# Optimization experiments

Hardware: AMD Instinct MI355X
Metric: run time of the kernel (lower is better)

Reference implementation:

```python
import jax, jax.numpy as jnp
import numpy as np

WS = (7, 7, 7)
SS = (3, 3, 3)
SEQ = WS[0] * WS[1] * WS[2]  # 343
EPS = 1e-5


def layer_norm(x, w, b):
    mu = jnp.mean(x, axis=-1, keepdims=True)
    var = jnp.mean((x - mu) ** 2, axis=-1, keepdims=True)
    return (x - mu) * jax.lax.rsqrt(var + EPS) * w + b


def window_partition(x, ws):
    b, d, h, w, c = x.shape
    x = x.reshape(b, d // ws[0], ws[0], h // ws[1], ws[1], w // ws[2], ws[2], c)
    return x.transpose(0, 1, 3, 5, 2, 4, 6, 7).reshape(-1, ws[0] * ws[1] * ws[2], c)


def window_reverse(win, ws, dims):
    b, dp, hp, wp = dims
    x = win.reshape(b, dp // ws[0], hp // ws[1], wp // ws[2], ws[0], ws[1], ws[2], -1)
    return x.transpose(0, 1, 4, 2, 5, 3, 6, 7).reshape(b, dp, hp, wp, -1)


def _rel_pos_index():
    coords = np.stack(np.meshgrid(np.arange(WS[0]), np.arange(WS[1]), np.arange(WS[2]), indexing='ij'))
    cf = coords.reshape(3, -1)
    rel = (cf[:, :, None] - cf[:, None, :]).transpose(1, 2, 0)  # (s, s, 3)
    rel[..., 0] += WS[0] - 1
    rel[..., 1] += WS[1] - 1
    rel[..., 2] += WS[2] - 1
    idx = rel[..., 0] * (2 * WS[1] - 1) * (2 * WS[2] - 1) + rel[..., 1] * (2 * WS[2] - 1) + rel[..., 2]
    return idx.astype(np.int32)


def _swin_mask(dp, hp, wp):
    img = np.zeros((1, dp, hp, wp, 1), np.float32)
    cnt = 0
    sl = lambda ws, ss: (slice(0, -ws), slice(-ws, -ss), slice(-ss, None))
    for ds in sl(WS[0], SS[0]):
        for hs in sl(WS[1], SS[1]):
            for wsl in sl(WS[2], SS[2]):
                img[:, ds, hs, wsl, :] = cnt
                cnt += 1
    mw = np.asarray(window_partition(jnp.asarray(img), WS)).squeeze(-1)  # (nW, s)
    am = mw[:, None, :] - mw[:, :, None]
    return np.where(am != 0, np.float32(-100.0), np.float32(0.0))


def setup_inputs() -> dict:
    key = jax.random.key(0)
    ks = jax.random.split(key, 12)
    B, D, H, W, C = 1, 28, 56, 28, 192
    NH, DH = 6, 32
    FFI = 4 * C
    L = 2
    s = 0.02
    inp = {
        'x': jax.random.normal(ks[0], (B, D, H, W, C), jnp.float32),
        'mask_matrix': jnp.asarray(_swin_mask(D, H, W)),
        'clinical': jax.random.normal(ks[1], (B, 8), jnp.float32),
        'ln1_w': jnp.ones((L, C)), 'ln1_b': jnp.zeros((L, C)),
        'qkv_w': jax.random.normal(ks[2], (L, C, 3 * C)) * s, 'qkv_b': jnp.zeros((L, 3 * C)),
        'out_w': jax.random.normal(ks[3], (L, C, C)) * s, 'out_b': jnp.zeros((L, C)),
        'ln2_w': jnp.ones((L, C)), 'ln2_b': jnp.zeros((L, C)),
        'ff1_w': jax.random.normal(ks[4], (L, C, 2 * FFI)) * s, 'ff1_b': jnp.zeros((L, 2 * FFI)),
        'ff2_w': jax.random.normal(ks[5], (L, FFI, C)) * s, 'ff2_b': jnp.zeros((L, C)),
        'rpb': jax.random.normal(ks[6], (L, (2 * WS[0] - 1) * (2 * WS[1] - 1) * (2 * WS[2] - 1), NH)) * s,
        'lnf_w': jnp.ones((C,)), 'lnf_b': jnp.zeros((C,)),
        'rel_index': jnp.asarray(_rel_pos_index()),
    }
    return inp


def reference(x, mask_matrix, clinical, ln1_w, ln1_b, qkv_w, qkv_b, out_w, out_b,
              ln2_w, ln2_b, ff1_w, ff1_b, ff2_w, ff2_b, rpb, lnf_w, lnf_b, rel_index):
    b, d, h, w, c = x.shape
    nh = rpb.shape[-1]
    dh = c // nh
    # pad to window multiples (no-op for chosen shapes, kept for fidelity)
    pd = (WS[0] - d % WS[0]) % WS[0]
    ph = (WS[1] - h % WS[1]) % WS[1]
    pw = (WS[2] - w % WS[2]) % WS[2]
    xp = jnp.pad(x, ((0, 0), (0, pd), (0, ph), (0, pw), (0, 0)))
    dp, hp, wp = d + pd, h + ph, w + pw
    # cyclic shift
    xs = jnp.roll(xp, shift=(-SS[0], -SS[1], -SS[2]), axis=(1, 2, 3))
    xw = window_partition(xs, WS)  # (nW*b, s, c)
    # mask: values {0,-100} -> allowed bool (True = attend), per source math
    allowed = jnp.logical_not((mask_matrix * (-1.0 / 100.0)).astype(bool))[:, None, :, :]
    scale = 1.0 / jnp.sqrt(jnp.asarray(dh, xw.dtype))
    for l in range(2):
        hdn = layer_norm(xw, ln1_w[l], ln1_b[l])
        qkv = hdn @ qkv_w[l] + qkv_b[l]
        q, k, v = jnp.split(qkv, 3, axis=-1)
        q = q.reshape(-1, SEQ, nh, dh).transpose(0, 2, 1, 3)
        k = k.reshape(-1, SEQ, nh, dh).transpose(0, 2, 1, 3)
        v = v.reshape(-1, SEQ, nh, dh).transpose(0, 2, 1, 3)
        scores = jnp.einsum('whqd,whkd->whqk', q, k) * scale
        bias = rpb[l][rel_index].transpose(2, 0, 1)  # (nh, s, s)
        scores = scores + bias[None]
        scores = jnp.where(allowed, scores, jnp.asarray(-1e9, scores.dtype))
        attn = jax.nn.softmax(scores, axis=-1)
        o = jnp.einsum('whqk,whkd->whqd', attn, v).transpose(0, 2, 1, 3).reshape(-1, SEQ, c)
        xw = xw + (o @ out_w[l] + out_b[l])
        f = layer_norm(xw, ln2_w[l], ln2_b[l]) @ ff1_w[l] + ff1_b[l]
        u, g = jnp.split(f, 2, axis=-1)  # GLU feed-forward
        xw = xw + ((u * jax.nn.gelu(g)) @ ff2_w[l] + ff2_b[l])
    xw = layer_norm(xw, lnf_w, lnf_b)
    aw = xw.reshape(-1, WS[0], WS[1], WS[2], c)
    xs = window_reverse(aw, WS, (b, dp, hp, wp))
    xo = jnp.roll(xs, shift=(SS[0], SS[1], SS[2]), axis=(1, 2, 3))
    return xo[:, :d, :h, :w, :]
```

## Files before the change

kernel.cpp:

```cpp
#include <hip/hip_runtime.h>
#include <hip/hip_fp16.h>
#include <math.h>

#define SEQ 343
#define CCH 192
#define NWIN 128
#define NHEAD 6
#define TOK (NWIN * SEQ)

typedef __bf16 bf16x8 __attribute__((ext_vector_type(8)));
typedef float f32x4 __attribute__((ext_vector_type(4)));
typedef unsigned short ushort8 __attribute__((ext_vector_type(8)));
typedef _Float16 half8 __attribute__((ext_vector_type(8)));
typedef _Float16 half4 __attribute__((ext_vector_type(4)));

__device__ __forceinline__ unsigned short f2bf(float f) {
    unsigned u = __float_as_uint(f);
    u += 0x7FFF + ((u >> 16) & 1);
    return (unsigned short)(u >> 16);
}

__device__ __forceinline__ float gelu_tanh(float x) {
    const float k0 = 0.7978845608028654f;
    const float k1 = 0.044715f;
    float t = tanhf(k0 * (x + k1 * x * x * x));
    return 0.5f * x * (1.0f + t);
}

__global__ __launch_bounds__(256) void k_shift_part(const float* __restrict__ x,
                                                    float* __restrict__ xw) {
    int idx = blockIdx.x * 256 + threadIdx.x;
    if (idx >= TOK * 48) return;
    int c4 = idx % 48;
    int tok = idx / 48;
    int t = tok % SEQ;
    int wn = tok / SEQ;
    int tw = t % 7, th = (t / 7) % 7, td = t / 49;
    int ww = wn & 3, wh = (wn >> 2) & 7, wd = wn >> 5;
    int sd = (wd * 7 + td + 3) % 28;
    int sh = (wh * 7 + th + 3) % 56;
    int sw = (ww * 7 + tw + 3) % 28;
    const float4* src = (const float4*)(x + (size_t)((sd * 56 + sh) * 28 + sw) * CCH);
    ((float4*)xw)[idx] = src[c4];
}

__global__ __launch_bounds__(256) void k_ln_bf(const float* __restrict__ in,
                                               const float* __restrict__ w,
                                               const float* __restrict__ b,
                                               unsigned short* __restrict__ out, int rows) {
    int row = blockIdx.x * 4 + (threadIdx.x >> 6);
    int lane = threadIdx.x & 63;
    if (row >= rows) return;
    const float* p = in + (size_t)row * CCH;
    float v0 = p[lane], v1 = p[lane + 64], v2 = p[lane + 128];
    float s = v0 + v1 + v2;
#pragma unroll
    for (int off = 32; off > 0; off >>= 1) s += __shfl_xor(s, off);
    float mu = s * (1.0f / 192.0f);
    float d0 = v0 - mu, d1 = v1 - mu, d2 = v2 - mu;
    float vv = d0 * d0 + d1 * d1 + d2 * d2;
#pragma unroll
    for (int off = 32; off > 0; off >>= 1) vv += __shfl_xor(vv, off);
    float rs = rsqrtf(vv * (1.0f / 192.0f) + 1e-5f);
    unsigned short* q = out + (size_t)row * CCH;
    q[lane] = f2bf(d0 * rs * w[lane] + b[lane]);
    q[lane + 64] = f2bf(d1 * rs * w[lane + 64] + b[lane + 64]);
    q[lane + 128] = f2bf(d2 * rs * w[lane + 128] + b[lane + 128]);
}

__global__ __launch_bounds__(256) void k_ln_out(const float* __restrict__ xw,
                                                const float* __restrict__ w,
                                                const float* __restrict__ b,
                                                float* __restrict__ out) {
    int row = blockIdx.x * 4 + (threadIdx.x >> 6);
    int lane = threadIdx.x & 63;
    if (row >= TOK) return;
    int d = row / 1568;
    int hh = (row / 28) % 56;
    int wv = row % 28;
    int sd = (d + 25) % 28, sh = (hh + 53) % 56, sw = (wv + 25) % 28;
    int wn = (sd / 7) * 32 + (sh / 7) * 4 + (sw / 7);
    int t = (sd % 7) * 49 + (sh % 7) * 7 + (sw % 7);
    const float* p = xw + ((size_t)wn * SEQ + t) * CCH;
    float v0 = p[lane], v1 = p[lane + 64], v2 = p[lane + 128];
    float s = v0 + v1 + v2;
#pragma unroll
    for (int off = 32; off > 0; off >>= 1) s += __shfl_xor(s, off);
    float mu = s * (1.0f / 192.0f);
    float d0 = v0 - mu, d1 = v1 - mu, d2 = v2 - mu;
    float vv = d0 * d0 + d1 * d1 + d2 * d2;
#pragma unroll
    for (int off = 32; off > 0; off >>= 1) vv += __shfl_xor(vv, off);
    float rs = rsqrtf(vv * (1.0f / 192.0f) + 1e-5f);
    float* q = out + (size_t)row * CCH;
    q[lane] = d0 * rs * w[lane] + b[lane];
    q[lane + 64] = d1 * rs * w[lane + 64] + b[lane + 64];
    q[lane + 128] = d2 * rs * w[lane + 128] + b[lane + 128];
}

__global__ __launch_bounds__(256) void k_wprep(const float* __restrict__ qkv_w,
                                               const float* __restrict__ out_w,
                                               const float* __restrict__ ff1_w,
                                               const float* __restrict__ ff2_w,
                                               unsigned short* __restrict__ wt) {
    int idx = blockIdx.x * 256 + threadIdx.x;
    if (idx >= 1179648) return;
    int l = idx / 589824;
    int r = idx - l * 589824;
    const float* src;
    int Kd, Nd, off;
    if (r < 110592)      { src = qkv_w + (size_t)l * 110592; Kd = 192; Nd = 576;  off = r; }
    else if (r < 147456) { src = out_w + (size_t)l * 36864;  Kd = 192; Nd = 192;  off = r - 110592; }
    else if (r < 442368) { src = ff1_w + (size_t)l * 294912; Kd = 192; Nd = 1536; off = r - 147456; }
    else                 { src = ff2_w + (size_t)l * 147456; Kd = 768; Nd = 192;  off = r - 442368; }
    int n = off / Kd, k = off - n * Kd;
    wt[idx] = f2bf(src[(size_t)k * Nd + n]);
}

__global__ void k_cbgen2(const float* __restrict__ mask, const float* __restrict__ rpb,
                         unsigned* __restrict__ cb) {
    int q = threadIdx.x;
    int kp = blockIdx.x;
    int h = blockIdx.y;
    int cl = blockIdx.z;
    int wn = ((cl & 4) ? 96 : 0) + ((cl & 2) ? 28 : 0) + ((cl & 1) ? 3 : 0);
    const float LOG2E = 1.4426950408889634f;
    int qd = q / 49, qh = (q / 7) % 7, qw = q % 7;
    unsigned short v[2];
#pragma unroll
    for (int t = 0; t < 2; ++t) {
        int k = 2 * kp + t;
        float val = -14000.0f;
        if (k < SEQ && q < SEQ) {
            float mk = mask[((size_t)wn * SEQ + k) * SEQ + q];
            if (mk == 0.0f) {
                int kd = k / 49, kh = (k / 7) % 7, kw = k % 7;
                int rel = (qd - kd + 6) * 169 + (qh - kh + 6) * 13 + (qw - kw + 6);
                val = rpb[(size_t)rel * NHEAD + h] * LOG2E;
            }
        }
        v[t] = __half_as_ushort(__float2half_rn(val));
    }
    cb[((size_t)(cl * NHEAD + h) * 176 + kp) * 352 + q] = (unsigned)v[0] | ((unsigned)v[1] << 16);
}

template <int MODE>
__global__ __launch_bounds__(256) void k_gemm_mfma(const unsigned short* __restrict__ A,
                                                   const unsigned short* __restrict__ Wt,
                                                   const float* __restrict__ bias,
                                                   float* __restrict__ outF,
                                                   unsigned short* __restrict__ outB,
                                                   _Float16* __restrict__ outH,
                                                   _Float16* __restrict__ outV,
                                                   int N, int K) {
    __shared__ unsigned short As[128][72];
    __shared__ unsigned short Bs[64][72];
    __shared__ unsigned short Bs2[(MODE == 2) ? 64 : 1][72];
    const int tid = threadIdx.x;
    const int n0 = blockIdx.x * 64;
    const size_t m0 = (size_t)blockIdx.y * 128;
    const int lane = tid & 63, wid = tid >> 6;
    const int wr = wid >> 1, wc = wid & 1;
    f32x4 acc[4][2];
    f32x4 acc2[4][2];
#pragma unroll
    for (int m = 0; m < 4; ++m)
#pragma unroll
        for (int n = 0; n < 2; ++n) {
            acc[m][n] = (f32x4){0.f, 0.f, 0.f, 0.f};
            acc2[m][n] = (f32x4){0.f, 0.f, 0.f, 0.f};
        }
    const int arow = wr * 64 + (lane & 15);
    const int bcol = wc * 32 + (lane & 15);
    const int kg = (lane >> 4) * 8;
    for (int kb = 0; kb < K; kb += 64) {
#pragma unroll
        for (int i = 0; i < 4; ++i) {
            int idx = tid + i * 256;
            int r = idx >> 3, ck = (idx & 7) << 3;
            *(ushort8*)&As[r][ck] = *(const ushort8*)&A[(m0 + r) * (size_t)K + kb + ck];
        }
#pragma unroll
        for (int i = 0; i < 2; ++i) {
            int idx = tid + i * 256;
            int r = idx >> 3, ck = (idx & 7) << 3;
            *(ushort8*)&Bs[r][ck] = *(const ushort8*)&Wt[(size_t)(n0 + r) * K + kb + ck];
            if (MODE == 2)
                *(ushort8*)&Bs2[r][ck] = *(const ushort8*)&Wt[(size_t)(N + n0 + r) * K + kb + ck];
        }
        __syncthreads();
#pragma unroll
        for (int kk = 0; kk < 64; kk += 32) {
            bf16x8 a[4], b[2];
#pragma unroll
            for (int m = 0; m < 4; ++m) a[m] = *(const bf16x8*)&As[arow + m * 16][kk + kg];
#pragma unroll
            for (int n = 0; n < 2; ++n) b[n] = *(const bf16x8*)&Bs[bcol + n * 16][kk + kg];
#pragma unroll
            for (int m = 0; m < 4; ++m)
#pragma unroll
                for (int n = 0; n < 2; ++n)
                    acc[m][n] = __builtin_amdgcn_mfma_f32_16x16x32_bf16(a[m], b[n], acc[m][n], 0, 0, 0);
            if (MODE == 2) {
                bf16x8 b2[2];
#pragma unroll
                for (int n = 0; n < 2; ++n) b2[n] = *(const bf16x8*)&Bs2[bcol + n * 16][kk + kg];
#pragma unroll
                for (int m = 0; m < 4; ++m)
#pragma unroll
                    for (int n = 0; n < 2; ++n)
                        acc2[m][n] = __builtin_amdgcn_mfma_f32_16x16x32_bf16(a[m], b2[n], acc2[m][n], 0, 0, 0);
            }
        }
        __syncthreads();
    }
    const float S2LOG = 0.17677669529663687f * 1.4426950408889634f;
    const int col0 = n0 + wc * 32 + (lane & 15);
    const int row0 = (int)m0 + wr * 64 + ((lane >> 4) << 2);
#pragma unroll
    for (int n = 0; n < 2; ++n) {
        int gc = col0 + n * 16;
        float bb = bias[gc];
        float bg = (MODE == 2) ? bias[N + gc] : 0.f;
#pragma unroll
        for (int m = 0; m < 4; ++m) {
            int gr = row0 + m * 16;
#pragma unroll
            for (int j = 0; j < 4; ++j) {
                float v = acc[m][n][j] + bb;
                size_t o = (size_t)(gr + j) * N + gc;
                if (MODE == 1) {
                    outF[o] += v;
                } else if (MODE == 2) {
                    float g = acc2[m][n][j] + bg;
                    outB[o] = f2bf(v * gelu_tanh(g));
                } else {
                    int rr = gr + j;
                    if (gc < 384) {
                        outH[(size_t)rr * 384 + gc] = (_Float16)(gc < 192 ? v * S2LOG : v);
                    } else {
                        int d = gc - 384;
                        int hh = d >> 5, dd = d & 31;
                        int wn_ = rr / 343, qq = rr - wn_ * 343;
                        outV[(((size_t)wn_ * NHEAD + hh) * 32 + dd) * 344 + qq] = (_Float16)v;
                    }
                }
            }
        }
    }
}

__global__ __launch_bounds__(256) void k_attn3(const _Float16* __restrict__ qk,
                                               const _Float16* __restrict__ vt,
                                               const unsigned* __restrict__ cb,
                                               unsigned short* __restrict__ o) {
    __shared__ _Float16 Ks[352][40];
    __shared__ _Float16 Vt[32][360];
    __shared__ _Float16 Pb[4][48][16][4];
    const int h = blockIdx.x;
    const int wn = blockIdx.y;
    const int tid = threadIdx.x;
    const _Float16* kbase = qk + (size_t)wn * SEQ * 384 + 192 + h * 32;
    for (int j = tid; j < 352 * 4; j += 256) {
        int s = j >> 2, c = (j & 3) * 8;
        half8 v = {};
        if (s < SEQ) v = *(const half8*)&kbase[(size_t)s * 384 + c];
        *(half8*)&Ks[s][c] = v;
    }
    const _Float16* vbase = vt + ((size_t)wn * NHEAD + h) * 32 * 344;
    for (int j = tid; j < 32 * 44; j += 256) {
        int d = j / 44, c = (j % 44) * 8;
        half8 v = {};
        if (c + 7 <= 342) {
            v = *(const half8*)&vbase[(size_t)d * 344 + c];
        } else if (c <= 342) {
#pragma unroll
            for (int i = 0; i < 8; ++i) v[i] = (c + i <= 342) ? vbase[(size_t)d * 344 + c + i] : (_Float16)0.f;
        }
        *(half8*)&Vt[d][c] = v;
    }
    __syncthreads();
    const int wid = tid >> 6, lane = tid & 63;
    const int qloc = lane & 15, g = lane >> 4;
    int cls = (((wn >> 5) == 3) ? 4 : 0) | ((((wn >> 2) & 7) == 7) ? 2 : 0) | (((wn & 3) == 3) ? 1 : 0);
    const unsigned* cbb = cb + (size_t)(cls * NHEAD + h) * 176 * 352;
    for (int qt = wid; qt < 22; qt += 4) {
        const int q0 = qt * 16;
        const int qrow = q0 + qloc;
        half8 qf = {};
        if (qrow < SEQ) qf = *(const half8*)&qk[((size_t)wn * SEQ + qrow) * 384 + h * 32 + g * 8];
        f32x4 st[22];
#pragma unroll
        for (int kt = 0; kt < 22; ++kt) {
            half8 kf = *(const half8*)&Ks[kt * 16 + qloc][g * 8];
            st[kt] = __builtin_amdgcn_mfma_f32_16x16x32_f16(kf, qf, (f32x4){0.f, 0.f, 0.f, 0.f}, 0, 0, 0);
        }
        float m = -1e30f;
#pragma unroll
        for (int kt = 0; kt < 22; ++kt) {
            const unsigned* cp = cbb + (size_t)(kt * 8 + g * 2) * 352 + q0 + qloc;
            unsigned b0 = cp[0];
            unsigned b1 = cp[352];
            __half2 h0 = *(__half2*)&b0, h1 = *(__half2*)&b1;
            st[kt][0] += __low2float(h0);
            st[kt][1] += __high2float(h0);
            st[kt][2] += __low2float(h1);
            st[kt][3] += __high2float(h1);
            m = fmaxf(m, fmaxf(fmaxf(st[kt][0], st[kt][1]), fmaxf(st[kt][2], st[kt][3])));
        }
        m = fmaxf(m, __shfl_xor(m, 16));
        m = fmaxf(m, __shfl_xor(m, 32));
        float l = 0.f;
        f32x4 acc0 = {0.f, 0.f, 0.f, 0.f}, acc1 = {0.f, 0.f, 0.f, 0.f};
        asm volatile("s_waitcnt lgkmcnt(0)" ::: "memory");
#pragma unroll
        for (int kt = 0; kt < 12; ++kt) {
            float p0 = exp2f(st[kt][0] - m), p1 = exp2f(st[kt][1] - m);
            float p2 = exp2f(st[kt][2] - m), p3 = exp2f(st[kt][3] - m);
            l += (p0 + p1) + (p2 + p3);
            half4 pv = {(_Float16)p0, (_Float16)p1, (_Float16)p2, (_Float16)p3};
            *(half4*)&Pb[wid][kt * 4 + g][qloc][0] = pv;
        }
        asm volatile("s_waitcnt lgkmcnt(0)" ::: "memory");
#pragma unroll
        for (int ks = 0; ks < 6; ++ks) {
            half4 pa = *(half4*)&Pb[wid][ks * 8 + g * 2][qloc][0];
            half4 pb = *(half4*)&Pb[wid][ks * 8 + g * 2 + 1][qloc][0];
            half8 pf = {pa[0], pa[1], pa[2], pa[3], pb[0], pb[1], pb[2], pb[3]};
            half8 v0 = *(const half8*)&Vt[qloc][ks * 32 + g * 8];
            half8 v1 = *(const half8*)&Vt[16 + qloc][ks * 32 + g * 8];
            acc0 = __builtin_amdgcn_mfma_f32_16x16x32_f16(v0, pf, acc0, 0, 0, 0);
            acc1 = __builtin_amdgcn_mfma_f32_16x16x32_f16(v1, pf, acc1, 0, 0, 0);
        }
        asm volatile("s_waitcnt lgkmcnt(0)" ::: "memory");
#pragma unroll
        for (int kt = 12; kt < 22; ++kt) {
            float p0 = exp2f(st[kt][0] - m), p1 = exp2f(st[kt][1] - m);
            float p2 = exp2f(st[kt][2] - m), p3 = exp2f(st[kt][3] - m);
            l += (p0 + p1) + (p2 + p3);
            half4 pv = {(_Float16)p0, (_Float16)p1, (_Float16)p2, (_Float16)p3};
            *(half4*)&Pb[wid][(kt - 12) * 4 + g][qloc][0] = pv;
        }
        asm volatile("s_waitcnt lgkmcnt(0)" ::: "memory");
#pragma unroll
        for (int ks = 0; ks < 5; ++ks) {
            half4 pa = *(half4*)&Pb[wid][ks * 8 + g * 2][qloc][0];
            half4 pb = *(half4*)&Pb[wid][ks * 8 + g * 2 + 1][qloc][0];
            half8 pf = {pa[0], pa[1], pa[2], pa[3], pb[0], pb[1], pb[2], pb[3]};
            half8 v0 = *(const half8*)&Vt[qloc][192 + ks * 32 + g * 8];
            half8 v1 = *(const half8*)&Vt[16 + qloc][192 + ks * 32 + g * 8];
            acc0 = __builtin_amdgcn_mfma_f32_16x16x32_f16(v0, pf, acc0, 0, 0, 0);
            acc1 = __builtin_amdgcn_mfma_f32_16x16x32_f16(v1, pf, acc1, 0, 0, 0);
        }
        l += __shfl_xor(l, 16);
        l += __shfl_xor(l, 32);
        if (qrow < SEQ) {
            float inv = 1.0f / l;
            unsigned short* orow = o + ((size_t)wn * SEQ + qrow) * CCH + h * 32;
            ushort2 w0 = {f2bf(acc0[0] * inv), f2bf(acc0[1] * inv)};
            ushort2 w1 = {f2bf(acc0[2] * inv), f2bf(acc0[3] * inv)};
            ushort2 w2 = {f2bf(acc1[0] * inv), f2bf(acc1[1] * inv)};
            ushort2 w3 = {f2bf(acc1[2] * inv), f2bf(acc1[3] * inv)};
            *(ushort2*)&orow[g * 4] = w0;
            *(ushort2*)&orow[g * 4 + 2] = w1;
            *(ushort2*)&orow[16 + g * 4] = w2;
            *(ushort2*)&orow[16 + g * 4 + 2] = w3;
        }
    }
}

extern "C" void kernel_launch(void* const* d_in, const int* in_sizes, int n_in,
                              void* d_out, int out_size, void* d_ws, size_t ws_size,
                              hipStream_t stream) {
    const float* x     = (const float*)d_in[0];
    const float* mask  = (const float*)d_in[1];
    const float* ln1_w = (const float*)d_in[3];
    const float* ln1_b = (const float*)d_in[4];
    const float* qkv_w = (const float*)d_in[5];
    const float* qkv_b = (const float*)d_in[6];
    const float* out_w = (const float*)d_in[7];
    const float* out_b = (const float*)d_in[8];
    const float* ln2_w = (const float*)d_in[9];
    const float* ln2_b = (const float*)d_in[10];
    const float* ff1_w = (const float*)d_in[11];
    const float* ff1_b = (const float*)d_in[12];
    const float* ff2_w = (const float*)d_in[13];
    const float* ff2_b = (const float*)d_in[14];
    const float* rpb   = (const float*)d_in[15];
    const float* lnf_w = (const float*)d_in[16];
    const float* lnf_b = (const float*)d_in[17];

    char* wsp = (char*)d_ws;
    float* xw = (float*)wsp;                          wsp += (size_t)TOK * 192 * 4;
    unsigned short* hdnb = (unsigned short*)wsp;      wsp += (size_t)TOK * 192 * 2;
    _Float16* qkh = (_Float16*)wsp;                   wsp += (size_t)TOK * 384 * 2;
    _Float16* vth = (_Float16*)wsp;                   wsp += (size_t)NWIN * NHEAD * 32 * 344 * 2;
    unsigned short* glub = (unsigned short*)wsp;      wsp += (size_t)TOK * 768 * 2;
    unsigned short* wt = (unsigned short*)wsp;        wsp += (size_t)1179648 * 2;
    unsigned* cb = (unsigned*)wsp;
    float* out = (float*)d_out;

    k_shift_part<<<8232, 256, 0, stream>>>(x, xw);
    k_wprep<<<4608, 256, 0, stream>>>(qkv_w, out_w, ff1_w, ff2_w, wt);
    for (int l = 0; l < 2; ++l) {
        unsigned short* wbase = wt + (size_t)l * 589824;
        k_cbgen2<<<dim3(176, NHEAD, 8), 352, 0, stream>>>(mask, rpb + (size_t)l * 2197 * NHEAD, cb);
        k_ln_bf<<<10976, 256, 0, stream>>>(xw, ln1_w + l * 192, ln1_b + l * 192, hdnb, TOK);
        k_gemm_mfma<3><<<dim3(9, 343), 256, 0, stream>>>(hdnb, wbase, qkv_b + l * 576,
                                                         nullptr, nullptr, qkh, vth, 576, 192);
        k_attn3<<<dim3(NHEAD, NWIN), 256, 0, stream>>>(qkh, vth, cb, hdnb);
        k_gemm_mfma<1><<<dim3(3, 343), 256, 0, stream>>>(hdnb, wbase + 110592, out_b + l * 192,
                                                         xw, nullptr, nullptr, nullptr, 192, 192);
        k_ln_bf<<<10976, 256, 0, stream>>>(xw, ln2_w + l * 192, ln2_b + l * 192, hdnb, TOK);
        k_gemm_mfma<2><<<dim3(12, 343), 256, 0, stream>>>(hdnb, wbase + 147456, ff1_b + l * 1536,
                                                          nullptr, glub, nullptr, nullptr, 768, 192);
        k_gemm_mfma<1><<<dim3(3, 343), 256, 0, stream>>>(glub, wbase + 442368, ff2_b + l * 192,
                                                         xw, nullptr, nullptr, nullptr, 192, 768);
    }
    k_ln_out<<<10976, 256, 0, stream>>>(xw, lnf_w, lnf_b, out);
}
```

Before: 600.7 us.

## Rewrite GEMMs with 32x32 MFMA, direct-to-LDS loads and XOR-swizzled shared tiles

Replaces the 16x16x32 MFMA GEMM with a 32x32x16 variant that loads global tiles straight into LDS via global_load_lds, using an XOR swizzle instead of padding to avoid bank conflicts. The QKV GEMM now uses 192-wide N tiles, so each block covers a whole q/k/v section and the grid is a third the size. GELU's tanh is replaced by an exp-based formula. The goal is less register and LDS traffic per MFMA and fewer redundant A-tile loads, at the cost of higher accumulator register pressure and slightly different GELU numerics.

```diff
diff --git a/kernel.cpp b/kernel.cpp
--- a/kernel.cpp
+++ b/kernel.cpp
@@ -10,6 +10,7 @@
 
 typedef __bf16 bf16x8 __attribute__((ext_vector_type(8)));
 typedef float f32x4 __attribute__((ext_vector_type(4)));
+typedef float f32x16 __attribute__((ext_vector_type(16)));
 typedef unsigned short ushort8 __attribute__((ext_vector_type(8)));
 typedef _Float16 half8 __attribute__((ext_vector_type(8)));
 typedef _Float16 half4 __attribute__((ext_vector_type(4)));
@@ -23,8 +24,14 @@
 __device__ __forceinline__ float gelu_tanh(float x) {
     const float k0 = 0.7978845608028654f;
     const float k1 = 0.044715f;
-    float t = tanhf(k0 * (x + k1 * x * x * x));
+    float y = k0 * (x + k1 * x * x * x);
+    float t = 1.0f - 2.0f / (__expf(2.0f * y) + 1.0f);
     return 0.5f * x * (1.0f + t);
+}
+
+__device__ __forceinline__ void gld16(void* l, const void* g) {
+    __builtin_amdgcn_global_load_lds((const __attribute__((address_space(1))) unsigned int*)g,
+                                     (__attribute__((address_space(3))) unsigned int*)l, 16, 0, 0);
 }
 
 __global__ __launch_bounds__(256) void k_shift_part(const float* __restrict__ x,
@@ -145,105 +152,107 @@
 }
 
 template <int MODE>
-__global__ __launch_bounds__(256) void k_gemm_mfma(const unsigned short* __restrict__ A,
-                                                   const unsigned short* __restrict__ Wt,
-                                                   const float* __restrict__ bias,
-                                                   float* __restrict__ outF,
-                                                   unsigned short* __restrict__ outB,
-                                                   _Float16* __restrict__ outH,
-                                                   _Float16* __restrict__ outV,
-                                                   int N, int K) {
-    __shared__ unsigned short As[128][72];
-    __shared__ unsigned short Bs[64][72];
-    __shared__ unsigned short Bs2[(MODE == 2) ? 64 : 1][72];
+__global__ __launch_bounds__(256) void k_gemm32(const unsigned short* __restrict__ A,
+                                                const unsigned short* __restrict__ Wt,
+                                                const float* __restrict__ bias,
+                                                float* __restrict__ outF,
+                                                unsigned short* __restrict__ outB,
+                                                _Float16* __restrict__ outH,
+                                                _Float16* __restrict__ outV,
+                                                int N, int K) {
+    constexpr int BN = (MODE == 0) ? 192 : 64;
+    constexpr int NF = (MODE == 0) ? 3 : 1;
+    constexpr int WNC = NF * 32;
+    constexpr int BROWS = (MODE == 0) ? 192 : ((MODE == 2) ? 128 : 64);
+    constexpr int BCH = (BROWS * 128) / 4096;
+    __shared__ char AsB[16384];
+    __shared__ char BsB[BROWS * 128];
     const int tid = threadIdx.x;
-    const int n0 = blockIdx.x * 64;
+    const int n0 = blockIdx.x * BN;
     const size_t m0 = (size_t)blockIdx.y * 128;
     const int lane = tid & 63, wid = tid >> 6;
-    const int wr = wid >> 1, wc = wid & 1;
-    f32x4 acc[4][2];
-    f32x4 acc2[4][2];
-#pragma unroll
-    for (int m = 0; m < 4; ++m)
-#pragma unroll
-        for (int n = 0; n < 2; ++n) {
-            acc[m][n] = (f32x4){0.f, 0.f, 0.f, 0.f};
-            acc2[m][n] = (f32x4){0.f, 0.f, 0.f, 0.f};
-        }
-    const int arow = wr * 64 + (lane & 15);
-    const int bcol = wc * 32 + (lane & 15);
-    const int kg = (lane >> 4) * 8;
+    const int wm = wid >> 1, wn = wid & 1;
+    const int ln31 = lane & 31, hi16 = (lane >> 5) * 16;
+    const int xorv = (ln31 & 7) << 4;
+    const size_t ldb = (size_t)K * 2;
+
+    f32x16 acc[2][NF];
+    f32x16 accG[2];
+#pragma unroll
+    for (int mi = 0; mi < 2; ++mi) {
+#pragma unroll
+        for (int nj = 0; nj < NF; ++nj) acc[mi][nj] = (f32x16)(0.f);
+        accG[mi] = (f32x16)(0.f);
+    }
+
     for (int kb = 0; kb < K; kb += 64) {
 #pragma unroll
         for (int i = 0; i < 4; ++i) {
-            int idx = tid + i * 256;
-            int r = idx >> 3, ck = (idx & 7) << 3;
-            *(ushort8*)&As[r][ck] = *(const ushort8*)&A[(m0 + r) * (size_t)K + kb + ck];
-        }
-#pragma unroll
-        for (int i = 0; i < 2; ++i) {
-            int idx = tid + i * 256;
-            int r = idx >> 3, ck = (idx & 7) << 3;
-            *(ushort8*)&Bs[r][ck] = *(const ushort8*)&Wt[(size_t)(n0 + r) * K + kb + ck];
-            if (MODE == 2)
-                *(ushort8*)&Bs2[r][ck] = *(const ushort8*)&Wt[(size_t)(N + n0 + r) * K + kb + ck];
+            int s = i * 4096 + tid * 16;
+            int r = s >> 7;
+            int cb = (s & 127) ^ ((r & 7) << 4);
+            gld16(AsB + s, (const char*)A + (m0 + r) * ldb + (size_t)kb * 2 + cb);
+        }
+#pragma unroll
+        for (int i = 0; i < BCH; ++i) {
+            int s = i * 4096 + tid * 16;
+            int r = s >> 7;
+            int cb = (s & 127) ^ ((r & 7) << 4);
+            int grow = n0 + r + ((MODE == 2 && r >= 64) ? 704 : 0);
+            gld16(BsB + s, (const char*)Wt + (size_t)grow * ldb + (size_t)kb * 2 + cb);
         }
         __syncthreads();
 #pragma unroll
-        for (int kk = 0; kk < 64; kk += 32) {
-            bf16x8 a[4], b[2];
-#pragma unroll
-            for (int m = 0; m < 4; ++m) a[m] = *(const bf16x8*)&As[arow + m * 16][kk + kg];
-#pragma unroll
-            for (int n = 0; n < 2; ++n) b[n] = *(const bf16x8*)&Bs[bcol + n * 16][kk + kg];
-#pragma unroll
-            for (int m = 0; m < 4; ++m)
-#pragma unroll
-                for (int n = 0; n < 2; ++n)
-                    acc[m][n] = __builtin_amdgcn_mfma_f32_16x16x32_bf16(a[m], b[n], acc[m][n], 0, 0, 0);
+        for (int ks = 0; ks < 4; ++ks) {
+            const int ccb = (ks * 32 + hi16) ^ xorv;
+            bf16x8 a0 = *(const bf16x8*)(AsB + (wm * 64 + ln31) * 128 + ccb);
+            bf16x8 a1 = *(const bf16x8*)(AsB + (wm * 64 + 32 + ln31) * 128 + ccb);
             if (MODE == 2) {
-                bf16x8 b2[2];
-#pragma unroll
-                for (int n = 0; n < 2; ++n) b2[n] = *(const bf16x8*)&Bs2[bcol + n * 16][kk + kg];
-#pragma unroll
-                for (int m = 0; m < 4; ++m)
-#pragma unroll
-                    for (int n = 0; n < 2; ++n)
-                        acc2[m][n] = __builtin_amdgcn_mfma_f32_16x16x32_bf16(a[m], b2[n], acc2[m][n], 0, 0, 0);
+                bf16x8 bu = *(const bf16x8*)(BsB + (wn * 32 + ln31) * 128 + ccb);
+                bf16x8 bg = *(const bf16x8*)(BsB + (64 + wn * 32 + ln31) * 128 + ccb);
+                acc[0][0] = __builtin_amdgcn_mfma_f32_32x32x16_bf16(a0, bu, acc[0][0], 0, 0, 0);
+                acc[1][0] = __builtin_amdgcn_mfma_f32_32x32x16_bf16(a1, bu, acc[1][0], 0, 0, 0);
+                accG[0] = __builtin_amdgcn_mfma_f32_32x32x16_bf16(a0, bg, accG[0], 0, 0, 0);
+                accG[1] = __builtin_amdgcn_mfma_f32_32x32x16_bf16(a1, bg, accG[1], 0, 0, 0);
+            } else {
+#pragma unroll
+                for (int nj = 0; nj < NF; ++nj) {
+                    bf16x8 b = *(const bf16x8*)(BsB + (wn * WNC + nj * 32 + ln31) * 128 + ccb);
+                    acc[0][nj] = __builtin_amdgcn_mfma_f32_32x32x16_bf16(a0, b, acc[0][nj], 0, 0, 0);
+                    acc[1][nj] = __builtin_amdgcn_mfma_f32_32x32x16_bf16(a1, b, acc[1][nj], 0, 0, 0);
+                }
             }
         }
         __syncthreads();
     }
+
     const float S2LOG = 0.17677669529663687f * 1.4426950408889634f;
-    const int col0 = n0 + wc * 32 + (lane & 15);
-    const int row0 = (int)m0 + wr * 64 + ((lane >> 4) << 2);
-#pragma unroll
-    for (int n = 0; n < 2; ++n) {
-        int gc = col0 + n * 16;
-        float bb = bias[gc];
-        float bg = (MODE == 2) ? bias[N + gc] : 0.f;
-#pragma unroll
-        for (int m = 0; m < 4; ++m) {
-            int gr = row0 + m * 16;
-#pragma unroll
-            for (int j = 0; j < 4; ++j) {
-                float v = acc[m][n][j] + bb;
-                size_t o = (size_t)(gr + j) * N + gc;
+    const int rbase = (int)m0 + wm * 64 + ((lane >> 5) << 2);
+    const int cbase = n0 + wn * WNC + ln31;
+#pragma unroll
+    for (int mi = 0; mi < 2; ++mi) {
+#pragma unroll
+        for (int nj = 0; nj < NF; ++nj) {
+            const int gc = cbase + nj * 32;
+            const float bb = bias[gc];
+            const float bgv = (MODE == 2) ? bias[768 + gc] : 0.f;
+#pragma unroll
+            for (int reg = 0; reg < 16; ++reg) {
+                const int row = rbase + mi * 32 + (reg & 3) + ((reg >> 2) << 3);
+                float v = acc[mi][nj][reg] + bb;
                 if (MODE == 1) {
-                    outF[o] += v;
-                } else if (MODE == 2) {
-                    float g = acc2[m][n][j] + bg;
-                    outB[o] = f2bf(v * gelu_tanh(g));
+                    outF[(size_t)row * N + gc] += v;
+                } else if (MODE == 0) {
+                    if (n0 < 384) {
+                        outH[(size_t)row * 384 + gc] = (_Float16)(n0 == 0 ? v * S2LOG : v);
+                    } else {
+                        int d = gc - 384, hh = d >> 5, dd = d & 31;
+                        int wnn = row / 343, qq = row - wnn * 343;
+                        outV[(((size_t)wnn * NHEAD + hh) * 32 + dd) * 344 + qq] = (_Float16)v;
+                    }
                 } else {
-                    int rr = gr + j;
-                    if (gc < 384) {
-                        outH[(size_t)rr * 384 + gc] = (_Float16)(gc < 192 ? v * S2LOG : v);
-                    } else {
-                        int d = gc - 384;
-                        int hh = d >> 5, dd = d & 31;
-                        int wn_ = rr / 343, qq = rr - wn_ * 343;
-                        outV[(((size_t)wn_ * NHEAD + hh) * 32 + dd) * 344 + qq] = (_Float16)v;
-                    }
+                    float g = accG[mi][reg] + bgv;
+                    outB[(size_t)row * 768 + gc] = f2bf(v * gelu_tanh(g));
                 }
             }
         }
@@ -406,16 +415,16 @@
         unsigned short* wbase = wt + (size_t)l * 589824;
         k_cbgen2<<<dim3(176, NHEAD, 8), 352, 0, stream>>>(mask, rpb + (size_t)l * 2197 * NHEAD, cb);
         k_ln_bf<<<10976, 256, 0, stream>>>(xw, ln1_w + l * 192, ln1_b + l * 192, hdnb, TOK);
-        k_gemm_mfma<3><<<dim3(9, 343), 256, 0, stream>>>(hdnb, wbase, qkv_b + l * 576,
-                                                         nullptr, nullptr, qkh, vth, 576, 192);
+        k_gemm32<0><<<dim3(3, 343), 256, 0, stream>>>(hdnb, wbase, qkv_b + l * 576,
+                                                      nullptr, nullptr, qkh, vth, 576, 192);
         k_attn3<<<dim3(NHEAD, NWIN), 256, 0, stream>>>(qkh, vth, cb, hdnb);
-        k_gemm_mfma<1><<<dim3(3, 343), 256, 0, stream>>>(hdnb, wbase + 110592, out_b + l * 192,
-                                                         xw, nullptr, nullptr, nullptr, 192, 192);
+        k_gemm32<1><<<dim3(3, 343), 256, 0, stream>>>(hdnb, wbase + 110592, out_b + l * 192,
+                                                      xw, nullptr, nullptr, nullptr, 192, 192);
         k_ln_bf<<<10976, 256, 0, stream>>>(xw, ln2_w + l * 192, ln2_b + l * 192, hdnb, TOK);
-        k_gemm_mfma<2><<<dim3(12, 343), 256, 0, stream>>>(hdnb, wbase + 147456, ff1_b + l * 1536,
-                                                          nullptr, glub, nullptr, nullptr, 768, 192);
-        k_gemm_mfma<1><<<dim3(3, 343), 256, 0, stream>>>(glub, wbase + 442368, ff2_b + l * 192,
-                                                         xw, nullptr, nullptr, nullptr, 192, 768);
+        k_gemm32<2><<<dim3(12, 343), 256, 0, stream>>>(hdnb, wbase + 147456, ff1_b + l * 1536,
+                                                       nullptr, glub, nullptr, nullptr, 768, 192);
+        k_gemm32<1><<<dim3(3, 343), 256, 0, stream>>>(glub, wbase + 442368, ff2_b + l * 192,
+                                                      xw, nullptr, nullptr, nullptr, 192, 768);
     }
     k_ln_out<<<10976, 256, 0, stream>>>(xw, lnf_w, lnf_b, out);
 }
```

After: 575.1 us. 4.3% less time.
